# Optimization experiments

Hardware: AMD Instinct MI355X
Metric: run time of the kernel (lower is better)

## Reference

```python
import jax, jax.numpy as jnp
import numpy as np
import math

D = 1024      # size_kernel
H = 16        # num_heads
HD = D // H   # head_dim
PAD = 1       # pad_index
B, S = 8, 1024


def setup_inputs() -> dict:
    key = jax.random.key(0)
    ks = jax.random.split(key, 10)
    scale = 1.0 / math.sqrt(D)
    x = jax.random.normal(ks[0], (B, S, D), dtype=jnp.float32)
    input_ids = jax.random.randint(ks[1], (B, S), 0, 10000, dtype=jnp.int64)
    Wq = jax.random.uniform(ks[2], (D, D), jnp.float32, -scale, scale)
    bq = jax.random.uniform(ks[3], (D,), jnp.float32, -scale, scale)
    Wk = jax.random.uniform(ks[4], (D, D), jnp.float32, -scale, scale)
    bk = jax.random.uniform(ks[5], (D,), jnp.float32, -scale, scale)
    Wv = jax.random.uniform(ks[6], (D, D), jnp.float32, -scale, scale)
    bv = jax.random.uniform(ks[7], (D,), jnp.float32, -scale, scale)
    Wo = jax.random.uniform(ks[8], (D, D), jnp.float32, -scale, scale)
    bo = jax.random.uniform(ks[9], (D,), jnp.float32, -scale, scale)
    return {"x": x, "input_ids": input_ids, "Wq": Wq, "bq": bq,
            "Wk": Wk, "bk": bk, "Wv": Wv, "bv": bv, "Wo": Wo, "bo": bo}


def reference(x, input_ids, Wq, bq, Wk, bk, Wv, bv, Wo, bo):
    b, s, _ = x.shape
    # QKV projections -> [b, h, s, hd]
    def split_heads(t):
        return t.reshape(b, s, H, HD).transpose(0, 2, 1, 3)
    q = split_heads(x @ Wq.T + bq)
    k = split_heads(x @ Wk.T + bk)
    v = split_heads(x @ Wv.T + bv)
    # scores [b, h, s, s]
    scores = jnp.einsum('bhqd,bhkd->bhqk', q, k) / math.sqrt(HD)
    pad_mask = (input_ids != PAD)[:, None, None, :]          # [b,1,1,s] keys
    causal = jnp.tril(jnp.ones((s, s), dtype=bool))[None, None]  # [1,1,s,s]
    mask = pad_mask & causal
    min_val = jnp.finfo(scores.dtype).min
    scores = jnp.where(mask, scores, min_val)
    attn = jax.nn.softmax(scores, axis=-1)
    out = jnp.einsum('bhqk,bhkd->bhqd', attn, v)             # [b,h,s,hd]
    out = out.transpose(0, 2, 1, 3).reshape(b, s, D)
    return out @ Wo.T + bo
```

## Files before the change

### kernel.cpp

```cpp
#include <hip/hip_runtime.h>

typedef __attribute__((ext_vector_type(8))) short bf16x8;
typedef __attribute__((ext_vector_type(8))) unsigned short u16x8;
typedef __attribute__((ext_vector_type(4))) unsigned short u16x4;
typedef __attribute__((ext_vector_type(4))) float f32x4;
typedef unsigned short u16t;

#define MFMA16(a, b, c) __builtin_amdgcn_mfma_f32_16x16x32_bf16((a), (b), (c), 0, 0, 0)
#define GLDS16(gp, lp)                                                        \
  __builtin_amdgcn_global_load_lds(                                           \
      (__attribute__((address_space(1))) void*)(gp),                          \
      (__attribute__((address_space(3))) void*)(lp), 16, 0, 0)

static constexpr float L2E = 1.44269504f;
static constexpr float MASKV = -1.0e30f;

__device__ __forceinline__ u16t f2b(float f) {
  unsigned u = __builtin_bit_cast(unsigned, f);
  u = u + 0x7fffu + ((u >> 16) & 1u);
  return (u16t)(u >> 16);
}

__global__ void cvt5(const float* __restrict__ x, const float* __restrict__ wq,
                     const float* __restrict__ wk, const float* __restrict__ wv,
                     const float* __restrict__ wo, u16t* __restrict__ xb,
                     u16t* __restrict__ wqb, u16t* __restrict__ wkb,
                     u16t* __restrict__ wvb, u16t* __restrict__ wob) {
  const int bid = blockIdx.x;
  const float* src; u16t* dst; int gb;
  if (bid < 4096)      { src = x;  dst = xb;  gb = bid; }
  else if (bid < 4608) { src = wq; dst = wqb; gb = bid - 4096; }
  else if (bid < 5120) { src = wk; dst = wkb; gb = bid - 4608; }
  else if (bid < 5632) { src = wv; dst = wvb; gb = bid - 5120; }
  else                 { src = wo; dst = wob; gb = bid - 5632; }
  const size_t i = (size_t)gb * 256 + threadIdx.x;
  const float4 a = ((const float4*)src)[2 * i];
  const float4 b = ((const float4*)src)[2 * i + 1];
  u16x8 r;
  r[0] = f2b(a.x); r[1] = f2b(a.y); r[2] = f2b(a.z); r[3] = f2b(a.w);
  r[4] = f2b(b.x); r[5] = f2b(b.y); r[6] = f2b(b.z); r[7] = f2b(b.w);
  *(u16x8*)&dst[8 * i] = r;
}

__global__ void gemm_qkv(const u16t* __restrict__ X,
                         const u16t* __restrict__ Wq, const u16t* __restrict__ Wk,
                         const u16t* __restrict__ Wv,
                         const float* __restrict__ bq, const float* __restrict__ bk,
                         const float* __restrict__ bv,
                         u16t* __restrict__ Qo, u16t* __restrict__ Ko,
                         u16t* __restrict__ Vo) {
  __shared__ __align__(16) u16t SMEM[24576];
  u16t* const As = SMEM;
  u16t* const Bs = SMEM + 8192;
  u16t* const Et = SMEM;

  const int t = threadIdx.x, lane = t & 63, w = t >> 6;
  const int wr = w >> 1, wc = w & 1, m = lane & 15, quad = lane >> 4;
  const int id = blockIdx.x;
  const int xcd = id & 7, j = id >> 3;
  const int by = xcd * 8 + (j & 7);
  const int rem = j >> 3;
  const int bx = rem & 7, z = rem >> 3;
  const int rowBase = by * 128, colBase = bx * 128;
  const u16t* W = (z == 0) ? Wq : ((z == 1) ? Wk : Wv);
  const float* bias = (z == 0) ? bq : ((z == 1) ? bk : bv);
  u16t* Out = (z == 0) ? Qo : ((z == 1) ? Ko : Vo);

  f32x4 acc[4][4];
#pragma unroll
  for (int i = 0; i < 4; i++)
#pragma unroll
    for (int j2 = 0; j2 < 4; j2++) acc[i][j2] = (f32x4){0.f, 0.f, 0.f, 0.f};

  const int lr = lane >> 2, lc = (lane & 3) * 8;
#pragma unroll
  for (int i = 0; i < 2; ++i) {
    const int r0 = i * 64 + w * 16;
    GLDS16(&X[(size_t)(rowBase + r0 + lr) * 1024 + lc], &As[r0 * 32]);
    GLDS16(&W[(size_t)(colBase + r0 + lr) * 1024 + lc], &Bs[r0 * 32]);
  }
  __syncthreads();

  for (int kt = 0; kt < 32; ++kt) {
    const int cur = kt & 1;
    if (kt < 31) {
#pragma unroll
      for (int i = 0; i < 2; ++i) {
        const int r0 = i * 64 + w * 16;
        GLDS16(&X[(size_t)(rowBase + r0 + lr) * 1024 + (kt + 1) * 32 + lc],
               &As[(cur ^ 1) * 4096 + r0 * 32]);
        GLDS16(&W[(size_t)(colBase + r0 + lr) * 1024 + (kt + 1) * 32 + lc],
               &Bs[(cur ^ 1) * 4096 + r0 * 32]);
      }
    }
    bf16x8 af[4], bfr[4];
#pragma unroll
    for (int i = 0; i < 4; i++)
      af[i] = *(const bf16x8*)&As[cur * 4096 + (wr * 64 + i * 16 + m) * 32 + quad * 8];
#pragma unroll
    for (int j2 = 0; j2 < 4; j2++)
      bfr[j2] = *(const bf16x8*)&Bs[cur * 4096 + (wc * 64 + j2 * 16 + m) * 32 + quad * 8];
#pragma unroll
    for (int i = 0; i < 4; i++)
#pragma unroll
      for (int j2 = 0; j2 < 4; j2++) acc[i][j2] = MFMA16(af[i], bfr[j2], acc[i][j2]);
    __syncthreads();
  }

  const int b_ = rowBase >> 10;
  const int sBase0 = rowBase & 1023;
  if (z == 2) {
    const int sBase = sBase0 + wr * 64;
#pragma unroll
    for (int j2 = 0; j2 < 4; j2++) {
      const int col = colBase + wc * 64 + j2 * 16 + m;
      const float bv_ = bias[col];
      const int h = col >> 6, hd = col & 63;
#pragma unroll
      for (int i = 0; i < 4; i++) {
        const int s0 = sBase + i * 16 + quad * 4;
        u16x4 pk;
#pragma unroll
        for (int r = 0; r < 4; r++) pk[r] = f2b(acc[i][j2][r] + bv_);
        *(u16x4*)&Out[(((size_t)b_ * 16 + h) * 64 + hd) * 1024 + s0] = pk;
      }
    }
  } else {
    constexpr int ESTR = 136;
#pragma unroll
    for (int j2 = 0; j2 < 4; j2++) {
      const int cl = wc * 64 + j2 * 16 + m;
      const float bv_ = bias[colBase + cl];
#pragma unroll
      for (int i = 0; i < 4; i++)
#pragma unroll
        for (int r = 0; r < 4; r++)
          Et[(wr * 64 + i * 16 + quad * 4 + r) * ESTR + cl] =
              f2b(acc[i][j2][r] + bv_);
    }
    __syncthreads();
    const int hbase = colBase >> 6;
#pragma unroll
    for (int it = 0; it < 8; ++it) {
      const int chunk = it * 256 + t;
      const int sl = chunk >> 4, c8 = chunk & 15;
      const u16x8 v = *(const u16x8*)&Et[sl * ESTR + c8 * 8];
      const int h2 = hbase + (c8 >> 3), hd0 = (c8 & 7) * 8;
      *(u16x8*)&Out[(((size_t)b_ * 16 + h2) * 1024 + (sBase0 + sl)) * 64 + hd0] = v;
    }
  }
}

__global__ void gemm_o(const u16t* __restrict__ A, const u16t* __restrict__ W,
                       const float* __restrict__ bias, float* __restrict__ Out) {
  __shared__ __align__(16) u16t As[2][128 * 32];
  __shared__ __align__(16) u16t Bs[2][128 * 32];
  const int t = threadIdx.x, lane = t & 63, w = t >> 6;
  const int wr = w >> 1, wc = w & 1, m = lane & 15, quad = lane >> 4;
  const int id = blockIdx.x;
  const int xcd = id & 7, j = id >> 3;
  const int by = xcd * 8 + (j & 7);
  const int bx = j >> 3;
  const int rowBase = by * 128, colBase = bx * 128;

  f32x4 acc[4][4];
#pragma unroll
  for (int i = 0; i < 4; i++)
#pragma unroll
    for (int j2 = 0; j2 < 4; j2++) acc[i][j2] = (f32x4){0.f, 0.f, 0.f, 0.f};

  const int lr = lane >> 2, lc = (lane & 3) * 8;
#pragma unroll
  for (int i = 0; i < 2; ++i) {
    const int r0 = i * 64 + w * 16;
    GLDS16(&A[(size_t)(rowBase + r0 + lr) * 1024 + lc], &As[0][r0 * 32]);
    GLDS16(&W[(size_t)(colBase + r0 + lr) * 1024 + lc], &Bs[0][r0 * 32]);
  }
  __syncthreads();

  for (int kt = 0; kt < 32; ++kt) {
    const int cur = kt & 1;
    if (kt < 31) {
#pragma unroll
      for (int i = 0; i < 2; ++i) {
        const int r0 = i * 64 + w * 16;
        GLDS16(&A[(size_t)(rowBase + r0 + lr) * 1024 + (kt + 1) * 32 + lc],
               &As[cur ^ 1][r0 * 32]);
        GLDS16(&W[(size_t)(colBase + r0 + lr) * 1024 + (kt + 1) * 32 + lc],
               &Bs[cur ^ 1][r0 * 32]);
      }
    }
    bf16x8 af[4], bfr[4];
#pragma unroll
    for (int i = 0; i < 4; i++)
      af[i] = *(const bf16x8*)&As[cur][(wr * 64 + i * 16 + m) * 32 + quad * 8];
#pragma unroll
    for (int j2 = 0; j2 < 4; j2++)
      bfr[j2] = *(const bf16x8*)&Bs[cur][(wc * 64 + j2 * 16 + m) * 32 + quad * 8];
#pragma unroll
    for (int i = 0; i < 4; i++)
#pragma unroll
      for (int j2 = 0; j2 < 4; j2++) acc[i][j2] = MFMA16(af[i], bfr[j2], acc[i][j2]);
    __syncthreads();
  }

#pragma unroll
  for (int j2 = 0; j2 < 4; j2++) {
    const int col = colBase + wc * 64 + j2 * 16 + m;
    const float bv_ = bias[col];
#pragma unroll
    for (int i = 0; i < 4; i++) {
#pragma unroll
      for (int r = 0; r < 4; r++) {
        const int row = rowBase + wr * 64 + i * 16 + quad * 4 + r;
        Out[(size_t)row * 1024 + col] = acc[i][j2][r] + bv_;
      }
    }
  }
}

__global__ __launch_bounds__(512) void attn(
    const u16t* __restrict__ Q, const u16t* __restrict__ K,
    const u16t* __restrict__ VT, const int* __restrict__ ids,
    u16t* __restrict__ Oo) {
  constexpr int PSTR = 72;
  __shared__ __align__(16) u16t Kb[2][64 * 64];
  __shared__ __align__(16) u16t Vb[2][64 * 64];
  __shared__ __align__(16) u16t Ps[8][16 * PSTR];
  __shared__ unsigned long long maskL[16];

  const int t = threadIdx.x, lane = t & 63, wl = t >> 6;
  const int m = lane & 15, quad = lane >> 4;
  const int id = blockIdx.x;
  const int g = id & 7, k_ = id >> 3;
  const int bh = g + 8 * (k_ & 15);
  const int p4 = k_ >> 4;
  const int b = bh >> 4, h = bh & 15;
  const size_t hoff = (size_t)bh * 65536;

  const int srow = lane >> 3;
  const int sg = (lane & 7) ^ (srow & 7);

#pragma unroll
  for (int c = 0; c < 2; ++c) {
    const int chunk = wl * 2 + c;
    const int idv = ids[b * 1024 + chunk * 64 + lane];
    const unsigned long long mk = __ballot(idv != 1);
    if (lane == 0) maskL[chunk] = mk;
  }
  __syncthreads();

  u16t* const Pw = &Ps[wl][0];

  for (int pass = 0; pass < 2; ++pass) {
    const int qt8 = pass ? (7 - p4) : p4;
    const int qbase = qt8 * 128 + wl * 16;
    const int qrow = qbase + m;
    const int ktmax = 2 * qt8 + 1;

    GLDS16(&K[hoff + (size_t)(wl * 8 + srow) * 64 + sg * 8], &Kb[0][wl * 512]);
    GLDS16(&VT[hoff + (size_t)(wl * 8 + srow) * 1024 + sg * 8], &Vb[0][wl * 512]);

    const bf16x8 qf0 =
        *(const bf16x8*)&Q[hoff + (size_t)(qbase + m) * 64 + quad * 8];
    const bf16x8 qf1 =
        *(const bf16x8*)&Q[hoff + (size_t)(qbase + m) * 64 + 32 + quad * 8];

    float mi = MASKV, li = 0.f;
    f32x4 o[4];
#pragma unroll
    for (int ot = 0; ot < 4; ot++) o[ot] = (f32x4){0.f, 0.f, 0.f, 0.f};

    __syncthreads();

    for (int kt = 0; kt <= ktmax; ++kt) {
      if (kt < ktmax) {
        u16t* const kb = &Kb[(kt + 1) & 1][wl * 512];
        u16t* const vb = &Vb[(kt + 1) & 1][wl * 512];
        GLDS16(&K[hoff + (size_t)((kt + 1) * 64 + wl * 8 + srow) * 64 + sg * 8], kb);
        GLDS16(&VT[hoff + (size_t)(wl * 8 + srow) * 1024 + (kt + 1) * 64 + sg * 8], vb);
      }

      if (kt * 64 <= qbase + 15) {
        const u16t* const Kc = Kb[kt & 1];
        const u16t* const Vc = Vb[kt & 1];

        const int dq0 = qrow - kt * 64;
        const int dqc = dq0 > 63 ? 63 : dq0;
        const unsigned long long causal =
            (dqc == 63) ? ~0ull : ((1ull << (dqc + 1)) - 1ull);
        const unsigned long long km2 = maskL[kt] & causal;
        const unsigned kqlo = (unsigned)(km2 >> (quad * 4));
        const unsigned kqhi = (unsigned)(km2 >> (quad * 4 + 32));

        f32x4 sc[4];
        float pm = MASKV;
#pragma unroll
        for (int nt = 0; nt < 4; nt++) {
          if ((kt * 64 + nt * 16) <= (qbase + 15)) {
            const int krow = (nt * 16 + m) * 64;
            const bf16x8 k0 =
                *(const bf16x8*)&Kc[krow + ((quad ^ (m & 7)) & 7) * 8];
            const bf16x8 k1 =
                *(const bf16x8*)&Kc[krow + (((quad + 4) ^ (m & 7)) & 7) * 8];
            f32x4 c = (f32x4){0.f, 0.f, 0.f, 0.f};
            c = MFMA16(k0, qf0, c);
            c = MFMA16(k1, qf1, c);
            const unsigned w32 = (nt < 2) ? kqlo : kqhi;
#pragma unroll
            for (int r = 0; r < 4; r++) {
              const int sh = (nt & 1) * 16 + r;
              const float s = ((w32 >> sh) & 1u) ? c[r] * 0.125f : MASKV;
              sc[nt][r] = s;
              pm = fmaxf(pm, s);
            }
          } else {
#pragma unroll
            for (int r = 0; r < 4; r++) sc[nt][r] = MASKV;
          }
        }
        pm = fmaxf(pm, __shfl_xor(pm, 16));
        pm = fmaxf(pm, __shfl_xor(pm, 32));

        if (__any(pm > mi + 8.0f)) {
          const float mn = (pm > mi + 8.0f) ? pm : mi;
          const float alpha = exp2f((mi - mn) * L2E);
          mi = mn;
          li *= alpha;
#pragma unroll
          for (int r = 0; r < 4; r++) {
            const float ar = __shfl(alpha, quad * 4 + r);
#pragma unroll
            for (int ot = 0; ot < 4; ot++) o[ot][r] *= ar;
          }
        }

        float rsum = 0.f;
#pragma unroll
        for (int nt = 0; nt < 4; nt++) {
          float pf[4];
#pragma unroll
          for (int r = 0; r < 4; r++) {
            pf[r] = exp2f((sc[nt][r] - mi) * L2E);
            rsum += pf[r];
          }
          unsigned w0, w1;
          asm("v_cvt_pk_bf16_f32 %0, %1, %2" : "=v"(w0) : "v"(pf[0]), "v"(pf[1]));
          asm("v_cvt_pk_bf16_f32 %0, %1, %2" : "=v"(w1) : "v"(pf[2]), "v"(pf[3]));
          uint2 wv; wv.x = w0; wv.y = w1;
          *(uint2*)&Pw[m * PSTR + nt * 16 + quad * 4] = wv;
        }
        rsum += __shfl_xor(rsum, 16);
        rsum += __shfl_xor(rsum, 32);
        li += rsum;

        const bf16x8 p0 = *(const bf16x8*)&Pw[m * PSTR + quad * 8];
        const bf16x8 p1 = *(const bf16x8*)&Pw[m * PSTR + 32 + quad * 8];
#pragma unroll
        for (int ot = 0; ot < 4; ot++) {
          const int vrow = (ot * 16 + m) * 64;
          const bf16x8 v0 =
              *(const bf16x8*)&Vc[vrow + ((quad ^ (m & 7)) & 7) * 8];
          const bf16x8 v1 =
              *(const bf16x8*)&Vc[vrow + (((quad + 4) ^ (m & 7)) & 7) * 8];
          o[ot] = MFMA16(p0, v0, o[ot]);
          o[ot] = MFMA16(p1, v1, o[ot]);
        }
      }

      __syncthreads();
    }

    const float linv = (li > 1e-30f) ? 1.f / li : 0.f;
#pragma unroll
    for (int r = 0; r < 4; r++) {
      const float inv = __shfl(linv, quad * 4 + r);
      const int qo = qbase + quad * 4 + r;
#pragma unroll
      for (int ot = 0; ot < 4; ot++) {
        const int col = h * 64 + ot * 16 + m;
        Oo[((size_t)(b * 1024 + qo)) * 1024 + col] = f2b(o[ot][r] * inv);
      }
    }
  }
}

extern "C" void kernel_launch(void* const* d_in, const int* in_sizes, int n_in,
                              void* d_out, int out_size, void* d_ws, size_t ws_size,
                              hipStream_t stream) {
  const float* x  = (const float*)d_in[0];
  const int*   ids = (const int*)d_in[1];
  const float* Wq = (const float*)d_in[2];
  const float* bq = (const float*)d_in[3];
  const float* Wk = (const float*)d_in[4];
  const float* bk = (const float*)d_in[5];
  const float* Wv = (const float*)d_in[6];
  const float* bv = (const float*)d_in[7];
  const float* Wo = (const float*)d_in[8];
  const float* bo = (const float*)d_in[9];
  float* out = (float*)d_out;

  u16t* XB  = (u16t*)d_ws;
  u16t* WqB = XB  + 8388608;
  u16t* WkB = WqB + 1048576;
  u16t* WvB = WkB + 1048576;
  u16t* WoB = WvB + 1048576;
  u16t* Qw  = WoB + 1048576;
  u16t* Kw  = Qw  + 8388608;
  u16t* Vw  = Kw  + 8388608;
  u16t* AO  = XB;

  cvt5<<<6144, 256, 0, stream>>>(x, Wq, Wk, Wv, Wo, XB, WqB, WkB, WvB, WoB);
  gemm_qkv<<<1536, 256, 0, stream>>>(XB, WqB, WkB, WvB, bq, bk, bv, Qw, Kw, Vw);
  attn<<<512, 512, 0, stream>>>(Qw, Kw, Vw, ids, AO);
  gemm_o<<<512, 256, 0, stream>>>(AO, WoB, bo, out);
}
```

Baseline: 242.2 us.

## Triple-buffer K/V tiles in attention with partial vmcnt waits

Moves the attention kernel from double to triple buffering of K and V tiles in LDS, prefetching two tiles ahead. The full __syncthreads drain becomes an explicit s_waitcnt vmcnt(2) plus s_barrier, so the next tile's loads can stay in flight across the barrier. The aim is to hide global-to-LDS latency better. It costs more LDS (another 16KB), which may cut occupancy, and its correctness relies on the vmcnt counting being exact, since any other outstanding global loads would break it.

New measurement: 246.2 us. Within noise of the previous version (+1.7%).

```diff
diff --git a/kernel.cpp b/kernel.cpp
--- a/kernel.cpp
+++ b/kernel.cpp
@@ -224,8 +224,8 @@
     const u16t* __restrict__ VT, const int* __restrict__ ids,
     u16t* __restrict__ Oo) {
   constexpr int PSTR = 72;
-  __shared__ __align__(16) u16t Kb[2][64 * 64];
-  __shared__ __align__(16) u16t Vb[2][64 * 64];
+  __shared__ __align__(16) u16t Kb[3][64 * 64];
+  __shared__ __align__(16) u16t Vb[3][64 * 64];
   __shared__ __align__(16) u16t Ps[8][16 * PSTR];
   __shared__ unsigned long long maskL[16];
 
@@ -260,6 +260,8 @@
 
     GLDS16(&K[hoff + (size_t)(wl * 8 + srow) * 64 + sg * 8], &Kb[0][wl * 512]);
     GLDS16(&VT[hoff + (size_t)(wl * 8 + srow) * 1024 + sg * 8], &Vb[0][wl * 512]);
+    GLDS16(&K[hoff + (size_t)(64 + wl * 8 + srow) * 64 + sg * 8], &Kb[1][wl * 512]);
+    GLDS16(&VT[hoff + (size_t)(wl * 8 + srow) * 1024 + 64 + sg * 8], &Vb[1][wl * 512]);
 
     const bf16x8 qf0 =
         *(const bf16x8*)&Q[hoff + (size_t)(qbase + m) * 64 + quad * 8];
@@ -271,19 +273,25 @@
 #pragma unroll
     for (int ot = 0; ot < 4; ot++) o[ot] = (f32x4){0.f, 0.f, 0.f, 0.f};
 
-    __syncthreads();
+    asm volatile("s_waitcnt vmcnt(2)" ::: "memory");
+    __builtin_amdgcn_sched_barrier(0);
+    __builtin_amdgcn_s_barrier();
+    __builtin_amdgcn_sched_barrier(0);
 
     for (int kt = 0; kt <= ktmax; ++kt) {
-      if (kt < ktmax) {
-        u16t* const kb = &Kb[(kt + 1) & 1][wl * 512];
-        u16t* const vb = &Vb[(kt + 1) & 1][wl * 512];
-        GLDS16(&K[hoff + (size_t)((kt + 1) * 64 + wl * 8 + srow) * 64 + sg * 8], kb);
-        GLDS16(&VT[hoff + (size_t)(wl * 8 + srow) * 1024 + (kt + 1) * 64 + sg * 8], vb);
+      const int cb = kt % 3;
+      const bool more = (kt + 2 <= ktmax);
+      if (more) {
+        const int nb = (kt + 2) % 3;
+        GLDS16(&K[hoff + (size_t)((kt + 2) * 64 + wl * 8 + srow) * 64 + sg * 8],
+               &Kb[nb][wl * 512]);
+        GLDS16(&VT[hoff + (size_t)(wl * 8 + srow) * 1024 + (kt + 2) * 64 + sg * 8],
+               &Vb[nb][wl * 512]);
       }
 
       if (kt * 64 <= qbase + 15) {
-        const u16t* const Kc = Kb[kt & 1];
-        const u16t* const Vc = Vb[kt & 1];
+        const u16t* const Kc = Kb[cb];
+        const u16t* const Vc = Vb[cb];
 
         const int dq0 = qrow - kt * 64;
         const int dqc = dq0 > 63 ? 63 : dq0;
@@ -368,7 +376,14 @@
         }
       }
 
-      __syncthreads();
+      if (more) {
+        asm volatile("s_waitcnt vmcnt(2)" ::: "memory");
+      } else {
+        asm volatile("s_waitcnt vmcnt(0)" ::: "memory");
+      }
+      __builtin_amdgcn_sched_barrier(0);
+      __builtin_amdgcn_s_barrier();
+      __builtin_amdgcn_sched_barrier(0);
     }
 
     const float linv = (li > 1e-30f) ? 1.f / li : 0.f;
```
